# Performance work log

Hardware: AMD Instinct MI355X
Metric: run time of the kernel (lower is better)

Reference implementation:

```python
import jax, jax.numpy as jnp
import numpy as np

P = 8        # patch (window) size
HEADS = 6
E = 192
HD = E // HEADS


def _layernorm(x, g, b, eps=1e-5):
    m = x.mean(-1, keepdims=True)
    v = ((x - m) ** 2).mean(-1, keepdims=True)
    return (x - m) / jnp.sqrt(v + eps) * g + b


def setup_inputs() -> dict:
    key = jax.random.key(0)
    ks = jax.random.split(key, 8)
    B, H, W = 8, 128, 128
    return {
        "x": jax.random.normal(ks[0], (B, E, H, W), jnp.float32),
        "row_embed": jax.random.uniform(ks[1], (P, E // 2), jnp.float32),
        "col_embed": jax.random.uniform(ks[2], (P, E // 2), jnp.float32),
        "ln1_g": jnp.ones((E,), jnp.float32),
        "ln1_b": jnp.zeros((E,), jnp.float32),
        "in_proj_w": jax.random.normal(ks[3], (3 * E, E), jnp.float32) * 0.02,
        "in_proj_b": jnp.zeros((3 * E,), jnp.float32),
        "out_w": jax.random.normal(ks[4], (E, E), jnp.float32) * 0.02,
        "out_b": jnp.zeros((E,), jnp.float32),
        "ln2_g": jnp.ones((E,), jnp.float32),
        "ln2_b": jnp.zeros((E,), jnp.float32),
        "ffn_w1": jax.random.normal(ks[5], (4 * E, E), jnp.float32) * 0.02,
        "ffn_b1": jnp.zeros((4 * E,), jnp.float32),
        "ffn_w2": jax.random.normal(ks[6], (E, 4 * E), jnp.float32) * 0.02,
        "ffn_b2": jnp.zeros((E,), jnp.float32),
    }


def reference(x, row_embed, col_embed, ln1_g, ln1_b, in_proj_w, in_proj_b,
              out_w, out_b, ln2_g, ln2_b, ffn_w1, ffn_b1, ffn_w2, ffn_b2):
    B, C, H, W = x.shape
    hp, wp = H // P, W // P
    # shift_size=0 and H,W multiples of P -> no roll, no padding, no mask.
    # to_patches: 'b c (hp p1) (wp p2) -> (p1 p2) (b hp wp) c'
    xp = (x.reshape(B, C, hp, P, wp, P)
           .transpose(3, 5, 0, 2, 4, 1)          # (p1, p2, B, hp, wp, C)
           .reshape(P * P, B * hp * wp, C))      # (L, N, C)
    # learnable positional embedding: (p^2, 1, E)
    pos = jnp.concatenate(
        [jnp.repeat(row_embed[:, None, :], P, axis=1),
         jnp.repeat(col_embed[None, :, :], P, axis=0)], axis=-1
    ).reshape(P * P, 1, C)
    xp = xp + pos
    residual = xp
    xn = _layernorm(xp, ln1_g, ln1_b)
    # self-attention (q = k = v = xn), torch MultiheadAttention math
    qkv = xn @ in_proj_w.T + in_proj_b            # (L, N, 3E)
    q, k, v = jnp.split(qkv, 3, axis=-1)
    L, N, _ = q.shape
    q = q.reshape(L, N, HEADS, HD)
    k = k.reshape(L, N, HEADS, HD)
    v = v.reshape(L, N, HEADS, HD)
    scale = 1.0 / jnp.sqrt(jnp.asarray(HD, jnp.float32))
    scores = jnp.einsum('lnhd,mnhd->nhlm', q * scale, k)   # (N, H, L, L)
    attn = jax.nn.softmax(scores, axis=-1)
    o = jnp.einsum('nhlm,mnhd->lnhd', attn, v).reshape(L, N, C)
    o = o @ out_w.T + out_b
    xp = o + residual
    # FFN (note: GELU after BOTH linears, per the source)
    h = _layernorm(xp, ln2_g, ln2_b)
    h = jax.nn.gelu(h @ ffn_w1.T + ffn_b1, approximate=False)
    h = jax.nn.gelu(h @ ffn_w2.T + ffn_b2, approximate=False)
    xp = xp + h
    # reverse rearrange: '(p1 p2) (b hp wp) c -> b c (hp p1) (wp p2)'
    out = (xp.reshape(P, P, B, hp, wp, C)
             .transpose(2, 5, 3, 0, 4, 1)        # (B, C, hp, p1, wp, p2)
             .reshape(B, C, H, W))
    return out
```

## Files before the change

### kernel.cpp

```cpp
#include <hip/hip_runtime.h>
#include <hip/hip_bf16.h>

typedef unsigned short u16;
typedef __bf16 bf16x8 __attribute__((ext_vector_type(8)));
typedef float f32x4 __attribute__((ext_vector_type(4)));

__device__ __forceinline__ u16 f2b(float f) {
  __hip_bfloat16 h = __float2bfloat16(f);
  return *reinterpret_cast<u16*>(&h);
}
__device__ __forceinline__ float gelu_f(float x) {
  return 0.5f * x * (1.0f + erff(x * 0.7071067811865475f));
}

__global__ __launch_bounds__(256) void k_cvt(const float* __restrict__ s, u16* __restrict__ d, int n) {
  int i = blockIdx.x * 256 + threadIdx.x;
  if (i < n) d[i] = f2b(s[i]);
}

__global__ __launch_bounds__(256) void k_patchify(const float* __restrict__ x,
                                                  const float* __restrict__ rowe,
                                                  const float* __restrict__ cole,
                                                  float* __restrict__ xp, int b0) {
  __shared__ float tile[64 * 129];
  const int cc = blockIdx.x, h = blockIdx.y, bb = blockIdx.z, b = b0 + bb;
  const int tid = threadIdx.x;
  const float* xs = x + ((size_t)(b * 192 + cc * 64) * 128 + h) * 128;
  for (int i = 0; i < 32; i++) {
    int idx = i * 256 + tid, r = idx >> 7, w = idx & 127;
    tile[r * 129 + w] = xs[(size_t)r * 16384 + w];
  }
  __syncthreads();
  const int p1 = h & 7, hy = h >> 3;
  const int c = tid & 63, cg = cc * 64 + c;
  for (int i = 0; i < 32; i++) {
    int w = i * 4 + (tid >> 6);
    int wx = w >> 3, p2 = w & 7;
    float pos = (cg < 96) ? rowe[p1 * 96 + cg] : cole[p2 * 96 + cg - 96];
    int rr = ((bb * 16 + hy) * 16 + wx) * 64 + p1 * 8 + p2;
    xp[(size_t)rr * 192 + cg] = tile[c * 129 + w] + pos;
  }
}

__global__ __launch_bounds__(256) void k_ln(const float* __restrict__ xin,
                                            const float* __restrict__ g,
                                            const float* __restrict__ bta,
                                            u16* __restrict__ outp) {
  const int wid = threadIdx.x >> 6, lane = threadIdx.x & 63;
  const size_t row = (size_t)blockIdx.x * 4 + wid;
  const float* p = xin + row * 192;
  float v0 = p[lane], v1 = p[lane + 64], v2 = p[lane + 128];
  float s = v0 + v1 + v2, q = v0 * v0 + v1 * v1 + v2 * v2;
  for (int m = 32; m >= 1; m >>= 1) { s += __shfl_xor(s, m, 64); q += __shfl_xor(q, m, 64); }
  float mean = s * (1.0f / 192.0f);
  float var = q * (1.0f / 192.0f) - mean * mean;
  float rstd = rsqrtf(var + 1e-5f);
  u16* o = outp + row * 192;
  o[lane]       = f2b((v0 - mean) * rstd * g[lane]       + bta[lane]);
  o[lane + 64]  = f2b((v1 - mean) * rstd * g[lane + 64]  + bta[lane + 64]);
  o[lane + 128] = f2b((v2 - mean) * rstd * g[lane + 128] + bta[lane + 128]);
}

enum { EP_BF16 = 0, EP_GELU_BF16 = 1, EP_RESID_F32 = 2, EP_GELU_ADD_F32 = 3 };

template <int EP, int KTOT>
__global__ __launch_bounds__(256, 2) void k_gemm(const u16* __restrict__ A,
                                                 const u16* __restrict__ W,
                                                 const float* __restrict__ bias,
                                                 const float* __restrict__ aux,
                                                 void* __restrict__ outp, int Nout) {
  __shared__ __align__(16) u16 ldsA[128 * 200];
  __shared__ __align__(16) u16 ldsB[64 * 200];
  const int tid = threadIdx.x;
  const int n0 = blockIdx.x * 64;
  const int m0 = blockIdx.y * 128;
  f32x4 acc[4][2] = {};
  const int lane = tid & 63, wid = tid >> 6;
  const int wm = wid >> 1, wn = wid & 1, lo = lane & 15, hi = lane >> 4;

  for (int kc = 0; kc < KTOT / 192; kc++) {
    if (kc) __syncthreads();
    for (int i = 0; i < 12; i++) {
      int gidx = i * 256 + tid, row = gidx / 24, kk = gidx % 24;
      uint4 d = *reinterpret_cast<const uint4*>(A + (size_t)(m0 + row) * KTOT + kc * 192 + kk * 8);
      *reinterpret_cast<uint4*>(&ldsA[row * 200 + kk * 8]) = d;
    }
    for (int i = 0; i < 6; i++) {
      int gidx = i * 256 + tid, row = gidx / 24, kk = gidx % 24;
      uint4 d = *reinterpret_cast<const uint4*>(W + (size_t)(n0 + row) * KTOT + kc * 192 + kk * 8);
      *reinterpret_cast<uint4*>(&ldsB[row * 200 + kk * 8]) = d;
    }
    __syncthreads();
    const u16* pa = &ldsA[(wm * 64 + lo) * 200 + hi * 8];
    const u16* pb = &ldsB[(wn * 32 + lo) * 200 + hi * 8];
#pragma unroll
    for (int kt = 0; kt < 6; kt++) {
      bf16x8 a[4], b[2];
#pragma unroll
      for (int mi = 0; mi < 4; mi++) a[mi] = *reinterpret_cast<const bf16x8*>(pa + mi * 16 * 200 + kt * 32);
#pragma unroll
      for (int ni = 0; ni < 2; ni++) b[ni] = *reinterpret_cast<const bf16x8*>(pb + ni * 16 * 200 + kt * 32);
#pragma unroll
      for (int mi = 0; mi < 4; mi++)
#pragma unroll
        for (int ni = 0; ni < 2; ni++)
          acc[mi][ni] = __builtin_amdgcn_mfma_f32_16x16x32_bf16(a[mi], b[ni], acc[mi][ni], 0, 0, 0);
    }
  }
#pragma unroll
  for (int mi = 0; mi < 4; mi++)
#pragma unroll
    for (int ni = 0; ni < 2; ni++) {
      int gn = n0 + wn * 32 + ni * 16 + lo;
      float bv = bias[gn];
#pragma unroll
      for (int r = 0; r < 4; r++) {
        int gm = m0 + wm * 64 + mi * 16 + hi * 4 + r;
        size_t oidx = (size_t)gm * Nout + gn;
        float v = acc[mi][ni][r] + bv;
        if (EP == EP_BF16)           ((u16*)outp)[oidx] = f2b(v);
        else if (EP == EP_GELU_BF16) ((u16*)outp)[oidx] = f2b(gelu_f(v));
        else if (EP == EP_RESID_F32) ((float*)outp)[oidx] = v + aux[oidx];
        else                         ((float*)outp)[oidx] = gelu_f(v) + aux[oidx];
      }
    }
}

__global__ __launch_bounds__(384) void k_attn(const u16* __restrict__ qkv, u16* __restrict__ o) {
  __shared__ __align__(16) u16 qk_lds[64 * 392];
  __shared__ __align__(16) u16 vt[192 * 72];
  __shared__ __align__(16) u16 pbuf[6 * 64 * 72];
  const int tid = threadIdx.x;
  const u16* src = qkv + (size_t)blockIdx.x * 64 * 576;
  for (int i = 0; i < 8; i++) {
    int g = i * 384 + tid, row = g / 48, kk = g % 48;
    uint4 d = *reinterpret_cast<const uint4*>(src + row * 576 + kk * 8);
    *reinterpret_cast<uint4*>(&qk_lds[row * 392 + kk * 8]) = d;
  }
  for (int i = 0; i < 4; i++) {
    int g = i * 384 + tid, row = g / 24, kk = g % 24;
    uint4 d = *reinterpret_cast<const uint4*>(src + row * 576 + 384 + kk * 8);
    const u16* ds = reinterpret_cast<const u16*>(&d);
#pragma unroll
    for (int e = 0; e < 8; e++) vt[(kk * 8 + e) * 72 + row] = ds[e];
  }
  __syncthreads();
  const int wid = tid >> 6, lane = tid & 63, lo = lane & 15, hi = lane >> 4;
  f32x4 s[4][4] = {};
  const u16* pq = &qk_lds[lo * 392 + wid * 32 + hi * 8];
  const u16* pk = &qk_lds[lo * 392 + 192 + wid * 32 + hi * 8];
  bf16x8 qa[4], kb[4];
#pragma unroll
  for (int mi = 0; mi < 4; mi++) qa[mi] = *reinterpret_cast<const bf16x8*>(pq + mi * 16 * 392);
#pragma unroll
  for (int nj = 0; nj < 4; nj++) kb[nj] = *reinterpret_cast<const bf16x8*>(pk + nj * 16 * 392);
#pragma unroll
  for (int mi = 0; mi < 4; mi++)
#pragma unroll
    for (int nj = 0; nj < 4; nj++)
      s[mi][nj] = __builtin_amdgcn_mfma_f32_16x16x32_bf16(qa[mi], kb[nj], s[mi][nj], 0, 0, 0);
  const float scale = 0.1767766952966369f;
#pragma unroll
  for (int mi = 0; mi < 4; mi++)
#pragma unroll
    for (int nj = 0; nj < 4; nj++)
#pragma unroll
      for (int r = 0; r < 4; r++) s[mi][nj][r] *= scale;
#pragma unroll
  for (int mi = 0; mi < 4; mi++)
#pragma unroll
    for (int r = 0; r < 4; r++) {
      float mx = fmaxf(fmaxf(s[mi][0][r], s[mi][1][r]), fmaxf(s[mi][2][r], s[mi][3][r]));
      mx = fmaxf(mx, __shfl_xor(mx, 1, 64));
      mx = fmaxf(mx, __shfl_xor(mx, 2, 64));
      mx = fmaxf(mx, __shfl_xor(mx, 4, 64));
      mx = fmaxf(mx, __shfl_xor(mx, 8, 64));
      float e0 = __expf(s[mi][0][r] - mx), e1 = __expf(s[mi][1][r] - mx);
      float e2 = __expf(s[mi][2][r] - mx), e3 = __expf(s[mi][3][r] - mx);
      float sm = e0 + e1 + e2 + e3;
      sm += __shfl_xor(sm, 1, 64);
      sm += __shfl_xor(sm, 2, 64);
      sm += __shfl_xor(sm, 4, 64);
      sm += __shfl_xor(sm, 8, 64);
      float inv = 1.0f / sm;
      int i = mi * 16 + hi * 4 + r;
      u16* pr = &pbuf[wid * 4608 + i * 72 + lo];
      pr[0]  = f2b(e0 * inv);
      pr[16] = f2b(e1 * inv);
      pr[32] = f2b(e2 * inv);
      pr[48] = f2b(e3 * inv);
    }
  f32x4 oacc[4][2] = {};
  const u16* pp = &pbuf[wid * 4608 + lo * 72 + hi * 8];
  const u16* pv = &vt[(wid * 32 + lo) * 72 + hi * 8];
#pragma unroll
  for (int kt = 0; kt < 2; kt++) {
    bf16x8 pa[4], vb[2];
#pragma unroll
    for (int mi = 0; mi < 4; mi++) pa[mi] = *reinterpret_cast<const bf16x8*>(pp + mi * 16 * 72 + kt * 32);
#pragma unroll
    for (int ni = 0; ni < 2; ni++) vb[ni] = *reinterpret_cast<const bf16x8*>(pv + ni * 16 * 72 + kt * 32);
#pragma unroll
    for (int mi = 0; mi < 4; mi++)
#pragma unroll
      for (int ni = 0; ni < 2; ni++)
        oacc[mi][ni] = __builtin_amdgcn_mfma_f32_16x16x32_bf16(pa[mi], vb[ni], oacc[mi][ni], 0, 0, 0);
  }
#pragma unroll
  for (int mi = 0; mi < 4; mi++)
#pragma unroll
    for (int ni = 0; ni < 2; ni++)
#pragma unroll
      for (int r = 0; r < 4; r++) {
        int i = mi * 16 + hi * 4 + r, d = ni * 16 + lo;
        o[((size_t)blockIdx.x * 64 + i) * 192 + wid * 32 + d] = f2b(oacc[mi][ni][r]);
      }
}

__global__ __launch_bounds__(256) void k_unpatch(const float* __restrict__ xf, float* __restrict__ outp, int b0) {
  __shared__ float tile[128 * 65];
  const int cc = blockIdx.x, h = blockIdx.y, bb = blockIdx.z, b = b0 + bb;
  const int tid = threadIdx.x;
  const int p1 = h & 7, hy = h >> 3;
  for (int i = 0; i < 32; i++) {
    int idx = i * 256 + tid, t = idx >> 6, c = idx & 63;
    int wx = t >> 3, p2 = t & 7;
    int rr = ((bb * 16 + hy) * 16 + wx) * 64 + p1 * 8 + p2;
    tile[t * 65 + c] = xf[(size_t)rr * 192 + cc * 64 + c];
  }
  __syncthreads();
  for (int i = 0; i < 32; i++) {
    int idx = i * 256 + tid, c = idx >> 7, w = idx & 127;
    outp[((size_t)(b * 192 + cc * 64 + c) * 128 + h) * 128 + w] = tile[w * 65 + c];
  }
}

extern "C" void kernel_launch(void* const* d_in, const int* in_sizes, int n_in,
                              void* d_out, int out_size, void* d_ws, size_t ws_size,
                              hipStream_t stream) {
  const float* x    = (const float*)d_in[0];
  const float* rowe = (const float*)d_in[1];
  const float* cole = (const float*)d_in[2];
  const float* ln1g = (const float*)d_in[3];
  const float* ln1b = (const float*)d_in[4];
  const float* ipw  = (const float*)d_in[5];
  const float* ipb  = (const float*)d_in[6];
  const float* outw = (const float*)d_in[7];
  const float* outb = (const float*)d_in[8];
  const float* ln2g = (const float*)d_in[9];
  const float* ln2b = (const float*)d_in[10];
  const float* w1   = (const float*)d_in[11];
  const float* b1   = (const float*)d_in[12];
  const float* w2   = (const float*)d_in[13];
  const float* b2   = (const float*)d_in[14];
  float* outp = (float*)d_out;

  char* p = (char*)d_ws;
  auto alloc = [&](size_t bytes) -> void* {
    void* r = (void*)p;
    p += (bytes + 255) & ~(size_t)255;
    return r;
  };
  u16* wq  = (u16*)alloc(110592 * 2);
  u16* wo  = (u16*)alloc(36864 * 2);
  u16* wf1 = (u16*)alloc(147456 * 2);
  u16* wf2 = (u16*)alloc(147456 * 2);

  size_t used = (size_t)(p - (char*)d_ws);
  size_t avail = (ws_size > used) ? (ws_size - used) : 0;
  int NC = 1;
  while (NC < 8 && (size_t)(131072 / NC) * 3840 + 8192 > avail) NC *= 2;
  const int Bc = 8 / NC;
  const size_t Mc = (size_t)Bc * 16384;

  float* resid = (float*)alloc(Mc * 192 * 4);
  u16*   xn    = (u16*)alloc(Mc * 192 * 2);
  u16*   big   = (u16*)alloc(Mc * 768 * 2);
  u16*   obuf  = (u16*)alloc(Mc * 192 * 2);
  float* xp2   = (float*)alloc(Mc * 192 * 4);
  float* xfin  = resid;

  k_cvt<<<dim3((110592 + 255) / 256), dim3(256), 0, stream>>>(ipw, wq, 110592);
  k_cvt<<<dim3((36864 + 255) / 256), dim3(256), 0, stream>>>(outw, wo, 36864);
  k_cvt<<<dim3((147456 + 255) / 256), dim3(256), 0, stream>>>(w1, wf1, 147456);
  k_cvt<<<dim3((147456 + 255) / 256), dim3(256), 0, stream>>>(w2, wf2, 147456);

  for (int ch = 0; ch < NC; ch++) {
    int b0 = ch * Bc;
    k_patchify<<<dim3(3, 128, Bc), dim3(256), 0, stream>>>(x, rowe, cole, resid, b0);
    k_ln<<<dim3((unsigned)(Mc / 4)), dim3(256), 0, stream>>>(resid, ln1g, ln1b, xn);
    k_gemm<EP_BF16, 192><<<dim3(9, (unsigned)(Mc / 128)), dim3(256), 0, stream>>>(xn, wq, ipb, nullptr, big, 576);
    k_attn<<<dim3((unsigned)(Bc * 256)), dim3(384), 0, stream>>>(big, obuf);
    k_gemm<EP_RESID_F32, 192><<<dim3(3, (unsigned)(Mc / 128)), dim3(256), 0, stream>>>(obuf, wo, outb, resid, xp2, 192);
    k_ln<<<dim3((unsigned)(Mc / 4)), dim3(256), 0, stream>>>(xp2, ln2g, ln2b, xn);
    k_gemm<EP_GELU_BF16, 192><<<dim3(12, (unsigned)(Mc / 128)), dim3(256), 0, stream>>>(xn, wf1, b1, nullptr, big, 768);
    k_gemm<EP_GELU_ADD_F32, 768><<<dim3(3, (unsigned)(Mc / 128)), dim3(256), 0, stream>>>(big, wf2, b2, xp2, xfin, 192);
    k_unpatch<<<dim3(3, 128, Bc), dim3(256), 0, stream>>>(xfin, outp, b0);
  }
}
```

Baseline: 808.3 us.

## Fuse patchify with LayerNorm1 and rewrite GEMM with direct global-to-LDS loads

Patchify and the first LayerNorm now run in one kernel. It stages all 192 channels of an image row in shared memory, computes per-token mean and variance there, and writes both the fp32 residual and the bf16 normalized activations. This removes a full round trip of the residual tensor through global memory. The GEMM is replaced by a version that moves operands straight from global memory into LDS with global_load_lds. It uses K chunks of 64, tile widths of 96 or 128 depending on the layer, and a higher occupancy hint. The tradeoffs are a large LDS footprint in the fused kernel, unpadded LDS rows that may cause bank conflicts, and more sync rounds per K chunk.

```diff
diff --git a/kernel.cpp b/kernel.cpp
--- a/kernel.cpp
+++ b/kernel.cpp
@@ -18,27 +18,65 @@
   if (i < n) d[i] = f2b(s[i]);
 }
 
-__global__ __launch_bounds__(256) void k_patchify(const float* __restrict__ x,
-                                                  const float* __restrict__ rowe,
-                                                  const float* __restrict__ cole,
-                                                  float* __restrict__ xp, int b0) {
-  __shared__ float tile[64 * 129];
-  const int cc = blockIdx.x, h = blockIdx.y, bb = blockIdx.z, b = b0 + bb;
+__global__ __launch_bounds__(256) void k_patchify_ln(const float* __restrict__ x,
+                                                     const float* __restrict__ rowe,
+                                                     const float* __restrict__ cole,
+                                                     const float* __restrict__ g,
+                                                     const float* __restrict__ bta,
+                                                     float* __restrict__ resid,
+                                                     u16* __restrict__ xn, int b0) {
+  __shared__ float tile[192 * 133];
+  __shared__ float ps[256], pq[256], mb[128], rb[128];
+  const int h = blockIdx.x, bb = blockIdx.y, b = b0 + bb;
   const int tid = threadIdx.x;
-  const float* xs = x + ((size_t)(b * 192 + cc * 64) * 128 + h) * 128;
-  for (int i = 0; i < 32; i++) {
-    int idx = i * 256 + tid, r = idx >> 7, w = idx & 127;
-    tile[r * 129 + w] = xs[(size_t)r * 16384 + w];
-  }
-  __syncthreads();
   const int p1 = h & 7, hy = h >> 3;
-  const int c = tid & 63, cg = cc * 64 + c;
-  for (int i = 0; i < 32; i++) {
-    int w = i * 4 + (tid >> 6);
+  const float* xs = x + ((size_t)b * 192 * 128 + (size_t)h) * 128;
+  for (int i = 0; i < 24; i++) {
+    int idx = i * 256 + tid;
+    int c = idx >> 5, w4 = idx & 31;
+    const float4 v = *reinterpret_cast<const float4*>(xs + (size_t)c * 16384 + w4 * 4);
+    float a0, a1, a2, a3;
+    if (c < 96) {
+      float pv = rowe[p1 * 96 + c];
+      a0 = a1 = a2 = a3 = pv;
+    } else {
+      int w = w4 * 4;
+      a0 = cole[((w)     & 7) * 96 + c - 96];
+      a1 = cole[((w + 1) & 7) * 96 + c - 96];
+      a2 = cole[((w + 2) & 7) * 96 + c - 96];
+      a3 = cole[((w + 3) & 7) * 96 + c - 96];
+    }
+    float* t = &tile[c * 133 + w4 * 4];
+    t[0] = v.x + a0; t[1] = v.y + a1; t[2] = v.z + a2; t[3] = v.w + a3;
+  }
+  __syncthreads();
+  {
+    int w = tid & 127, half = tid >> 7;
+    float s = 0.f, q = 0.f;
+    for (int c = half * 96; c < half * 96 + 96; c++) {
+      float v = tile[c * 133 + w];
+      s += v; q += v * v;
+    }
+    ps[tid] = s; pq[tid] = q;
+  }
+  __syncthreads();
+  if (tid < 128) {
+    float s = ps[tid] + ps[tid + 128];
+    float q = pq[tid] + pq[tid + 128];
+    float mean = s * (1.f / 192.f);
+    float var = q * (1.f / 192.f) - mean * mean;
+    mb[tid] = mean;
+    rb[tid] = rsqrtf(var + 1e-5f);
+  }
+  __syncthreads();
+  for (int i = 0; i < 96; i++) {
+    int idx = i * 256 + tid;
+    int w = idx / 192, c = idx - w * 192;
+    float v = tile[c * 133 + w];
     int wx = w >> 3, p2 = w & 7;
-    float pos = (cg < 96) ? rowe[p1 * 96 + cg] : cole[p2 * 96 + cg - 96];
-    int rr = ((bb * 16 + hy) * 16 + wx) * 64 + p1 * 8 + p2;
-    xp[(size_t)rr * 192 + cg] = tile[c * 129 + w] + pos;
+    size_t rr = ((size_t)((bb * 16 + hy) * 16 + wx)) * 64 + p1 * 8 + p2;
+    resid[rr * 192 + c] = v;
+    xn[rr * 192 + c] = f2b((v - mb[w]) * rb[w] * g[c] + bta[c]);
   }
 }
 
@@ -63,61 +101,80 @@
 
 enum { EP_BF16 = 0, EP_GELU_BF16 = 1, EP_RESID_F32 = 2, EP_GELU_ADD_F32 = 3 };
 
-template <int EP, int KTOT>
-__global__ __launch_bounds__(256, 2) void k_gemm(const u16* __restrict__ A,
-                                                 const u16* __restrict__ W,
-                                                 const float* __restrict__ bias,
-                                                 const float* __restrict__ aux,
-                                                 void* __restrict__ outp, int Nout) {
-  __shared__ __align__(16) u16 ldsA[128 * 200];
-  __shared__ __align__(16) u16 ldsB[64 * 200];
+template <int BN, int EP, int KTOT>
+__global__ __launch_bounds__(256, 3) void k_gemm2(const u16* __restrict__ A,
+                                                  const u16* __restrict__ W,
+                                                  const float* __restrict__ bias,
+                                                  const float* __restrict__ aux,
+                                                  void* __restrict__ outp, int Nout) {
+  constexpr int NF = BN / 32;
+  constexpr int NBS = BN / 32;
+  __shared__ __align__(16) u16 ldsA[128 * 64];
+  __shared__ __align__(16) u16 ldsB[BN * 64];
   const int tid = threadIdx.x;
-  const int n0 = blockIdx.x * 64;
+  const int lane = tid & 63, wid = tid >> 6;
+  const int lo = lane & 15, hi = lane >> 4;
+  const int wm = wid >> 1, wn = wid & 1;
+  const int n0 = blockIdx.x * BN;
   const int m0 = blockIdx.y * 128;
-  f32x4 acc[4][2] = {};
-  const int lane = tid & 63, wid = tid >> 6;
-  const int wm = wid >> 1, wn = wid & 1, lo = lane & 15, hi = lane >> 4;
-
-  for (int kc = 0; kc < KTOT / 192; kc++) {
+
+  const int lrow = lane >> 3, lk = (lane & 7) * 8;
+  const u16* agp[4];
+  const u16* bgp[NBS];
+  u16* alp[4];
+  u16* blp[NBS];
+#pragma unroll
+  for (int i = 0; i < 4; i++) {
+    agp[i] = A + (size_t)(m0 + i * 32 + wid * 8 + lrow) * KTOT + lk;
+    alp[i] = ldsA + (i * 4 + wid) * 512;
+  }
+#pragma unroll
+  for (int i = 0; i < NBS; i++) {
+    bgp[i] = W + (size_t)(n0 + i * 32 + wid * 8 + lrow) * KTOT + lk;
+    blp[i] = ldsB + (i * 4 + wid) * 512;
+  }
+
+  f32x4 acc[4][NF] = {};
+  for (int kc = 0; kc < KTOT / 64; kc++) {
     if (kc) __syncthreads();
-    for (int i = 0; i < 12; i++) {
-      int gidx = i * 256 + tid, row = gidx / 24, kk = gidx % 24;
-      uint4 d = *reinterpret_cast<const uint4*>(A + (size_t)(m0 + row) * KTOT + kc * 192 + kk * 8);
-      *reinterpret_cast<uint4*>(&ldsA[row * 200 + kk * 8]) = d;
-    }
-    for (int i = 0; i < 6; i++) {
-      int gidx = i * 256 + tid, row = gidx / 24, kk = gidx % 24;
-      uint4 d = *reinterpret_cast<const uint4*>(W + (size_t)(n0 + row) * KTOT + kc * 192 + kk * 8);
-      *reinterpret_cast<uint4*>(&ldsB[row * 200 + kk * 8]) = d;
-    }
+#pragma unroll
+    for (int i = 0; i < 4; i++)
+      __builtin_amdgcn_global_load_lds(
+          (const __attribute__((address_space(1))) void*)(agp[i] + kc * 64),
+          (__attribute__((address_space(3))) void*)alp[i], 16, 0, 0);
+#pragma unroll
+    for (int i = 0; i < NBS; i++)
+      __builtin_amdgcn_global_load_lds(
+          (const __attribute__((address_space(1))) void*)(bgp[i] + kc * 64),
+          (__attribute__((address_space(3))) void*)blp[i], 16, 0, 0);
     __syncthreads();
-    const u16* pa = &ldsA[(wm * 64 + lo) * 200 + hi * 8];
-    const u16* pb = &ldsB[(wn * 32 + lo) * 200 + hi * 8];
-#pragma unroll
-    for (int kt = 0; kt < 6; kt++) {
-      bf16x8 a[4], b[2];
-#pragma unroll
-      for (int mi = 0; mi < 4; mi++) a[mi] = *reinterpret_cast<const bf16x8*>(pa + mi * 16 * 200 + kt * 32);
-#pragma unroll
-      for (int ni = 0; ni < 2; ni++) b[ni] = *reinterpret_cast<const bf16x8*>(pb + ni * 16 * 200 + kt * 32);
+#pragma unroll
+    for (int kt = 0; kt < 2; kt++) {
+      bf16x8 a[4], b[NF];
 #pragma unroll
       for (int mi = 0; mi < 4; mi++)
-#pragma unroll
-        for (int ni = 0; ni < 2; ni++)
-          acc[mi][ni] = __builtin_amdgcn_mfma_f32_16x16x32_bf16(a[mi], b[ni], acc[mi][ni], 0, 0, 0);
-    }
-  }
-#pragma unroll
-  for (int mi = 0; mi < 4; mi++)
-#pragma unroll
-    for (int ni = 0; ni < 2; ni++) {
-      int gn = n0 + wn * 32 + ni * 16 + lo;
+        a[mi] = *reinterpret_cast<const bf16x8*>(&ldsA[(wm * 64 + mi * 16 + lo) * 64 + kt * 32 + hi * 8]);
+#pragma unroll
+      for (int nj = 0; nj < NF; nj++)
+        b[nj] = *reinterpret_cast<const bf16x8*>(&ldsB[(wn * (BN / 2) + nj * 16 + lo) * 64 + kt * 32 + hi * 8]);
+#pragma unroll
+      for (int mi = 0; mi < 4; mi++)
+#pragma unroll
+        for (int nj = 0; nj < NF; nj++)
+          acc[mi][nj] = __builtin_amdgcn_mfma_f32_16x16x32_bf16(a[mi], b[nj], acc[mi][nj], 0, 0, 0);
+    }
+  }
+#pragma unroll
+  for (int mi = 0; mi < 4; mi++)
+#pragma unroll
+    for (int nj = 0; nj < NF; nj++) {
+      int gn = n0 + wn * (BN / 2) + nj * 16 + lo;
       float bv = bias[gn];
 #pragma unroll
       for (int r = 0; r < 4; r++) {
         int gm = m0 + wm * 64 + mi * 16 + hi * 4 + r;
         size_t oidx = (size_t)gm * Nout + gn;
-        float v = acc[mi][ni][r] + bv;
+        float v = acc[mi][nj][r] + bv;
         if (EP == EP_BF16)           ((u16*)outp)[oidx] = f2b(v);
         else if (EP == EP_GELU_BF16) ((u16*)outp)[oidx] = f2b(gelu_f(v));
         else if (EP == EP_RESID_F32) ((float*)outp)[oidx] = v + aux[oidx];
@@ -133,12 +190,12 @@
   const int tid = threadIdx.x;
   const u16* src = qkv + (size_t)blockIdx.x * 64 * 576;
   for (int i = 0; i < 8; i++) {
-    int g = i * 384 + tid, row = g / 48, kk = g % 48;
+    int gq = i * 384 + tid, row = gq / 48, kk = gq % 48;
     uint4 d = *reinterpret_cast<const uint4*>(src + row * 576 + kk * 8);
     *reinterpret_cast<uint4*>(&qk_lds[row * 392 + kk * 8]) = d;
   }
   for (int i = 0; i < 4; i++) {
-    int g = i * 384 + tid, row = g / 24, kk = g % 24;
+    int gq = i * 384 + tid, row = gq / 24, kk = gq % 24;
     uint4 d = *reinterpret_cast<const uint4*>(src + row * 576 + 384 + kk * 8);
     const u16* ds = reinterpret_cast<const u16*>(&d);
 #pragma unroll
@@ -287,14 +344,13 @@
 
   for (int ch = 0; ch < NC; ch++) {
     int b0 = ch * Bc;
-    k_patchify<<<dim3(3, 128, Bc), dim3(256), 0, stream>>>(x, rowe, cole, resid, b0);
-    k_ln<<<dim3((unsigned)(Mc / 4)), dim3(256), 0, stream>>>(resid, ln1g, ln1b, xn);
-    k_gemm<EP_BF16, 192><<<dim3(9, (unsigned)(Mc / 128)), dim3(256), 0, stream>>>(xn, wq, ipb, nullptr, big, 576);
+    k_patchify_ln<<<dim3(128, Bc), dim3(256), 0, stream>>>(x, rowe, cole, ln1g, ln1b, resid, xn, b0);
+    k_gemm2<96, EP_BF16, 192><<<dim3(6, (unsigned)(Mc / 128)), dim3(256), 0, stream>>>(xn, wq, ipb, nullptr, big, 576);
     k_attn<<<dim3((unsigned)(Bc * 256)), dim3(384), 0, stream>>>(big, obuf);
-    k_gemm<EP_RESID_F32, 192><<<dim3(3, (unsigned)(Mc / 128)), dim3(256), 0, stream>>>(obuf, wo, outb, resid, xp2, 192);
+    k_gemm2<96, EP_RESID_F32, 192><<<dim3(2, (unsigned)(Mc / 128)), dim3(256), 0, stream>>>(obuf, wo, outb, resid, xp2, 192);
     k_ln<<<dim3((unsigned)(Mc / 4)), dim3(256), 0, stream>>>(xp2, ln2g, ln2b, xn);
-    k_gemm<EP_GELU_BF16, 192><<<dim3(12, (unsigned)(Mc / 128)), dim3(256), 0, stream>>>(xn, wf1, b1, nullptr, big, 768);
-    k_gemm<EP_GELU_ADD_F32, 768><<<dim3(3, (unsigned)(Mc / 128)), dim3(256), 0, stream>>>(big, wf2, b2, xp2, xfin, 192);
+    k_gemm2<128, EP_GELU_BF16, 192><<<dim3(6, (unsigned)(Mc / 128)), dim3(256), 0, stream>>>(xn, wf1, b1, nullptr, big, 768);
+    k_gemm2<96, EP_GELU_ADD_F32, 768><<<dim3(2, (unsigned)(Mc / 128)), dim3(256), 0, stream>>>(big, wf2, b2, xp2, xfin, 192);
     k_unpatch<<<dim3(3, 128, Bc), dim3(256), 0, stream>>>(xfin, outp, b0);
   }
 }
```

New measurement: 855.2 us. 5.8% more time.
